# Performance work log

Measured on AMD Instinct MI355X. Metric: run time of the kernel, lower is better.

The kernel has to match this reference:

```python
import jax, jax.numpy as jnp
import numpy as np

B, S, H = 4, 2048, 1024
DECAY_RATE = 0.5  # MemoryModule decay: exp(-decay_rate * k), k=1 (most recent pattern)


def setup_inputs() -> dict:
    key = jax.random.key(0)
    ks = jax.random.split(key, 7)
    hidden_states = jax.random.normal(ks[0], (B, S, H), dtype=jnp.float32)
    # past attention pattern: valid row-stochastic attention probs [B, S, S]
    pa = jax.random.uniform(ks[1], (B, S, S), dtype=jnp.float32)
    past_attention = pa / pa.sum(-1, keepdims=True)
    scale = 1.0 / np.sqrt(H).astype(np.float32)
    Wq = jax.random.normal(ks[2], (H, H), dtype=jnp.float32) * scale
    Wk = jax.random.normal(ks[3], (H, H), dtype=jnp.float32) * scale
    Wv = jax.random.normal(ks[4], (H, H), dtype=jnp.float32) * scale
    Wm = jax.random.normal(ks[5], (H, H), dtype=jnp.float32) * scale
    w_gate = jax.random.normal(ks[6], (H,), dtype=jnp.float32) * scale
    return {"hidden_states": hidden_states, "past_attention": past_attention,
            "Wq": Wq, "Wk": Wk, "Wv": Wv, "Wm": Wm, "w_gate": w_gate}


def reference(hidden_states, past_attention, Wq, Wk, Wv, Wm, w_gate):
    h = hidden_states.shape[-1]
    inv_sqrt_h = 1.0 / (h ** 0.5)
    # QKV projections (hidden -> hidden)
    q = jnp.einsum('bsh,hd->bsd', hidden_states, Wq)
    k = jnp.einsum('bsh,hd->bsd', hidden_states, Wk)
    v = jnp.einsum('bsh,hd->bsd', hidden_states, Wv)
    # base attention scores QK^T / sqrt(H)
    scores = jnp.einsum('bqd,bkd->bqk', q, k) * inv_sqrt_h
    # --- memory bias ---
    # decayed history pattern (single most-recent entry, k=1)
    memory = past_attention * jnp.exp(jnp.float32(-DECAY_RATE * 1.0))  # [B,S,S]
    # per-token scalar gate from query
    gates = jax.nn.sigmoid(jnp.einsum('bsh,h->bs', q, w_gate))  # [B,S]
    memory_values = jnp.einsum('bqk,bkd->bqd', memory, v)        # memory @ V
    transformed = jnp.einsum('bsh,hd->bsd', memory_values, Wm)   # memory_transform (no bias)
    gated_memory = gates[..., None] * transformed
    memory_bias = jnp.einsum('bqd,bkd->bqk', gated_memory, k) * inv_sqrt_h
    # augmented attention
    probs = jax.nn.softmax(scores + memory_bias, axis=-1)
    context = jnp.einsum('bqk,bkd->bqd', probs, v)
    return context
```

## Files before the change

kernel.cpp:

```cpp
#include <hip/hip_runtime.h>
#include <hip/hip_bf16.h>

typedef __attribute__((ext_vector_type(4))) float f32x4;
typedef __attribute__((ext_vector_type(8))) __bf16 bf16x8;

__device__ __forceinline__ unsigned short f2bf(float f) {
    union { float f; unsigned u; } x; x.f = f;
    unsigned r = x.u + 0x7fffu + ((x.u >> 16) & 1u);
    return (unsigned short)(r >> 16);
}
__device__ __forceinline__ float bf2f(unsigned short b) {
    union { unsigned u; float f; } x; x.u = ((unsigned)b) << 16;
    return x.f;
}

__device__ __forceinline__ void gload16(const void* g, void* l) {
    __builtin_amdgcn_global_load_lds(
        (const __attribute__((address_space(1))) unsigned int*)g,
        (__attribute__((address_space(3))) unsigned int*)l,
        16, 0, 0);
}

template <int N> __device__ __forceinline__ void vm_wait();
template <> __device__ __forceinline__ void vm_wait<0>() { asm volatile("s_waitcnt vmcnt(0)" ::: "memory"); }
template <> __device__ __forceinline__ void vm_wait<2>() { asm volatile("s_waitcnt vmcnt(2)" ::: "memory"); }
template <> __device__ __forceinline__ void vm_wait<4>() { asm volatile("s_waitcnt vmcnt(4)" ::: "memory"); }

__global__ __launch_bounds__(256) void k_wg2(const float* __restrict__ Wq,
                                             const float* __restrict__ wg,
                                             float* __restrict__ wg2) {
    int lane = threadIdx.x & 63;
    int row = blockIdx.x * 4 + (threadIdx.x >> 6);
    const float4* a = reinterpret_cast<const float4*>(Wq + (size_t)row * 1024);
    const float4* x = reinterpret_cast<const float4*>(wg);
    float s = 0.f;
    for (int i = lane; i < 256; i += 64) {
        float4 av = a[i], bv = x[i];
        s += av.x * bv.x + av.y * bv.y + av.z * bv.z + av.w * bv.w;
    }
#pragma unroll
    for (int o = 1; o < 64; o <<= 1) s += __shfl_xor(s, o);
    if (lane == 0) wg2[row] = s;
}

__global__ __launch_bounds__(256) void k_prep(
    const float* __restrict__ hs, const float* __restrict__ pa,
    const float* __restrict__ Wq, const float* __restrict__ Wk,
    const float* __restrict__ Wv, const float* __restrict__ Wm,
    unsigned short* __restrict__ hs_bf, unsigned short* __restrict__ pa_bf,
    unsigned short* __restrict__ WT, float decay,
    const float* __restrict__ wg2, float* __restrict__ gates) {
    __shared__ float tile[32][33];
    __shared__ float red[4];
    unsigned b = blockIdx.x;
    int t = threadIdx.x;
    if (b < 16384u) {
        int i = b * 256 + t;
        float4 v = reinterpret_cast<const float4*>(pa)[i];
        union { unsigned short u[4]; uint2 q; } o;
        o.u[0] = f2bf(v.x * decay); o.u[1] = f2bf(v.y * decay);
        o.u[2] = f2bf(v.z * decay); o.u[3] = f2bf(v.w * decay);
        reinterpret_cast<uint2*>(pa_bf)[i] = o.q;
    } else if (b < 24576u) {
        unsigned row = b - 16384u;
        int i = row * 256 + t;
        float4 v = reinterpret_cast<const float4*>(hs)[i];
        union { unsigned short u[4]; uint2 q; } o;
        o.u[0] = f2bf(v.x); o.u[1] = f2bf(v.y);
        o.u[2] = f2bf(v.z); o.u[3] = f2bf(v.w);
        reinterpret_cast<uint2*>(hs_bf)[i] = o.q;
        float4 w = reinterpret_cast<const float4*>(wg2)[t];
        float s = v.x * w.x + v.y * w.y + v.z * w.z + v.w * w.w;
#pragma unroll
        for (int o2 = 1; o2 < 64; o2 <<= 1) s += __shfl_xor(s, o2);
        if ((t & 63) == 0) red[t >> 6] = s;
        __syncthreads();
        if (t == 0) {
            float ss = red[0] + red[1] + red[2] + red[3];
            gates[row] = 1.f / (1.f + __expf(-ss));
        }
    } else {
        unsigned bb = b - 24576u;
        int z = bb >> 10, rem = bb & 1023;
        int bx = rem & 31, by = rem >> 5;
        const float* src = z == 0 ? Wq : z == 1 ? Wk : z == 2 ? Wv : Wm;
        unsigned short* dst = WT + (size_t)z * 1024 * 1024;
        int lx = t & 31, ly8 = t >> 5;
        int x = bx * 32 + lx;
#pragma unroll
        for (int i = 0; i < 4; i++)
            tile[ly8 + i * 8][lx] = src[(size_t)(by * 32 + ly8 + i * 8) * 1024 + x];
        __syncthreads();
        int tx = by * 32 + lx;
#pragma unroll
        for (int i = 0; i < 4; i++)
            dst[(size_t)(bx * 32 + ly8 + i * 8) * 1024 + tx] = f2bf(tile[lx][ly8 + i * 8]);
    }
}

template <int BN>
struct Geo {
    static constexpr int WN = BN / 64;
    static constexpr int WM = 8 / WN;
    static constexpr int WROWS = 256 / WM;
    static constexpr int MF = WROWS / 16;
    static constexpr int MP = MF / 4;
    static constexpr int ASZ = 256 * 64 * 2;
    static constexpr int BSZ = BN * 64 * 2;
    static constexpr int BUFSZ = ASZ + BSZ;
};

#define GPH(BUFOFF, MB, LB, STG, VMW)                                                   \
    {                                                                                   \
        const char* aB = smem + (BUFOFF);                                               \
        const char* bB = aB + G::ASZ;                                                   \
        bf16x8 af[G::MP * 2];                                                           \
        _Pragma("unroll") for (int mm = 0; mm < G::MP; ++mm)                            \
        _Pragma("unroll") for (int kk = 0; kk < 2; ++kk) {                              \
            int rowx = wrow + ((MB) + mm) * 16 + fr;                                    \
            int slot = (kk * 4 + kq) ^ (rowx & 7);                                      \
            af[mm * 2 + kk] = *reinterpret_cast<const bf16x8*>(aB + rowx * 128 + slot * 16); \
        }                                                                               \
        if (LB) {                                                                       \
            _Pragma("unroll") for (int nn = 0; nn < 4; ++nn)                            \
            _Pragma("unroll") for (int kk = 0; kk < 2; ++kk) {                          \
                int rowx = wcol + nn * 16 + fr;                                         \
                int slot = (kk * 4 + kq) ^ (rowx & 7);                                  \
                bfrag[nn * 2 + kk] = *reinterpret_cast<const bf16x8*>(bB + rowx * 128 + slot * 16); \
            }                                                                           \
        }                                                                               \
        STG;                                                                            \
        __builtin_amdgcn_sched_barrier(0);                                              \
        VMW;                                                                            \
        __builtin_amdgcn_s_barrier();                                                   \
        asm volatile("s_waitcnt lgkmcnt(0)" ::: "memory");                              \
        __builtin_amdgcn_sched_barrier(0);                                              \
        __builtin_amdgcn_s_setprio(1);                                                  \
        _Pragma("unroll") for (int mm = 0; mm < G::MP; ++mm)                            \
        _Pragma("unroll") for (int nn = 0; nn < 4; ++nn)                                \
        _Pragma("unroll") for (int kk = 0; kk < 2; ++kk)                                \
            acc[(MB) + mm][nn] = __builtin_amdgcn_mfma_f32_16x16x32_bf16(               \
                af[mm * 2 + kk], bfrag[nn * 2 + kk], acc[(MB) + mm][nn], 0, 0, 0);      \
        __builtin_amdgcn_s_setprio(0);                                                  \
        __builtin_amdgcn_sched_barrier(0);                                              \
        __builtin_amdgcn_s_barrier();                                                   \
        __builtin_amdgcn_sched_barrier(0);                                              \
    }

template <int EPI, int BN>
__device__ __forceinline__ void gemm_body(
    char* smem,
    const unsigned short* __restrict__ A, int ldA, long long bsA,
    const unsigned short* __restrict__ Bt, int ldB, long long bsB,
    void* __restrict__ Cv, int ldC, long long bsC,
    const unsigned short* __restrict__ Qm, int ldQ,
    const float* __restrict__ gates, float alpha, int K,
    int NX, int NY, int NB, int yf) {
    using G = Geo<BN>;
    const int NT = K >> 6, NI = K >> 7;

    unsigned b = blockIdx.x;
    unsigned wg = (b & 7) * (gridDim.x >> 3) + (b >> 3);
    int xT, yT, zB;
    if (yf) {
        yT = wg % NY; unsigned r2 = wg / NY;
        xT = r2 % NX; zB = (int)(r2 / NX) % NB;
    } else {
        xT = wg % NX; unsigned r2 = wg / NX;
        yT = r2 % NY; zB = (int)(r2 / NY) % NB;
    }

    const unsigned short* Ab = A + (size_t)zB * (size_t)bsA;
    const unsigned short* Bb = Bt + (size_t)zB * (size_t)bsB;

    int t = threadIdx.x, lane = t & 63, wave = t >> 6;
    int wc = wave % G::WN, wr = wave / G::WN;
    int fr = lane & 15, kq = lane >> 4;
    int wrow = wr * G::WROWS, wcol = wc * 64;
    int trow = t >> 3, csx = (t & 7) ^ (trow & 7);
    long long rowTile = (long long)yT * 256, colTile = (long long)xT * BN;

    f32x4 acc[G::MF][4];
#pragma unroll
    for (int m = 0; m < G::MF; ++m)
#pragma unroll
        for (int n = 0; n < 4; ++n) acc[m][n] = (f32x4){0.f, 0.f, 0.f, 0.f};
    bf16x8 bfrag[8];

    auto stageA = [&](int buf, int h, int tt) {
        int kt = tt < NT ? tt : NT - 1;
#pragma unroll
        for (int rr = 0; rr < 2; ++rr) {
            const unsigned short* src =
                Ab + (size_t)(rowTile + h * 128 + rr * 64 + trow) * (size_t)ldA + kt * 64 + csx * 8;
            gload16(src, smem + buf * G::BUFSZ + h * 16384 + rr * 8192 + t * 16);
        }
    };
    auto stageB = [&](int buf, int h, int tt) {
        int kt = tt < NT ? tt : NT - 1;
        if (BN == 256) {
#pragma unroll
            for (int rr = 0; rr < 2; ++rr) {
                const unsigned short* src =
                    Bb + (size_t)(colTile + h * 128 + rr * 64 + trow) * (size_t)ldB + kt * 64 + csx * 8;
                gload16(src, smem + buf * G::BUFSZ + G::ASZ + h * 16384 + rr * 8192 + t * 16);
            }
        } else {
            const unsigned short* src =
                Bb + (size_t)(colTile + h * 64 + trow) * (size_t)ldB + kt * 64 + csx * 8;
            gload16(src, smem + buf * G::BUFSZ + G::ASZ + h * 8192 + t * 16);
        }
    };

    stageA(0, 0, 0); stageA(0, 1, 0);
    stageB(0, 0, 0); stageB(0, 1, 0);
    stageB(1, 0, 1); stageB(1, 1, 1);
    __builtin_amdgcn_sched_barrier(0);
    vm_wait<0>();
    __builtin_amdgcn_s_barrier();
    __builtin_amdgcn_sched_barrier(0);

    constexpr int VMN = (BN == 256) ? 4 : 2;
    for (int i = 0; i < NI; ++i) {
        int t1 = 2 * i + 1, t2 = 2 * i + 2, t3 = 2 * i + 3;
        GPH(0,          0,         1, stageA(1, 0, t1), (void)0);
        GPH(0,          G::MP,     0, stageA(1, 1, t1), (void)0);
        GPH(0,          2 * G::MP, 0, stageB(0, 0, t2), (void)0);
        GPH(0,          3 * G::MP, 0, stageB(0, 1, t2), vm_wait<VMN>());
        GPH(G::BUFSZ,   0,         1, stageA(0, 0, t2), (void)0);
        GPH(G::BUFSZ,   G::MP,     0, stageA(0, 1, t2), (void)0);
        GPH(G::BUFSZ,   2 * G::MP, 0, stageB(1, 0, t3), (void)0);
        GPH(G::BUFSZ,   3 * G::MP, 0, stageB(1, 1, t3), vm_wait<VMN>());
    }
    vm_wait<0>();

    long long rb0 = rowTile + wrow + kq * 4;
    long long cb0 = colTile + wcol + fr;
    if (EPI == 0) {
        unsigned short* C = (unsigned short*)Cv + (size_t)zB * (size_t)bsC;
#pragma unroll
        for (int m = 0; m < G::MF; ++m)
#pragma unroll
            for (int n = 0; n < 4; ++n)
#pragma unroll
                for (int r = 0; r < 4; ++r)
                    C[(size_t)(rb0 + m * 16 + r) * (size_t)ldC + cb0 + n * 16] =
                        f2bf(acc[m][n][r] * alpha);
    } else if (EPI == 1) {
        unsigned short* C = (unsigned short*)Cv;
#pragma unroll
        for (int m = 0; m < G::MF; ++m)
#pragma unroll
            for (int r = 0; r < 4; ++r) {
                long long row = rb0 + m * 16 + r;
                float g = gates[row];
#pragma unroll
                for (int n = 0; n < 4; ++n) {
                    long long col = cb0 + n * 16;
                    float v = (bf2f(Qm[(size_t)row * (size_t)ldQ + col]) + g * acc[m][n][r]) * alpha;
                    C[(size_t)row * (size_t)ldC + col] = f2bf(v);
                }
            }
    } else if (EPI == 4) {
        float* C = (float*)Cv + (size_t)zB * (size_t)bsC;
#pragma unroll
        for (int m = 0; m < G::MF; ++m)
#pragma unroll
            for (int r = 0; r < 4; ++r) {
                long long row = rb0 + m * 16 + r;
                const float4* pp = reinterpret_cast<const float4*>(
                    gates + ((size_t)zB * 2048 + row) * 8);
                float4 p0 = pp[0], p1 = pp[1];
                float g = 1.f / (p0.x + p0.y + p0.z + p0.w + p1.x + p1.y + p1.z + p1.w);
#pragma unroll
                for (int n = 0; n < 4; ++n)
                    C[(size_t)row * (size_t)ldC + cb0 + n * 16] = acc[m][n][r] * g;
            }
    } else if (EPI == 5) {
        unsigned short* C = (unsigned short*)Cv + (size_t)zB * (size_t)bsC;
        float* partials = (float*)gates;
        float srow[G::MF][4];
#pragma unroll
        for (int m = 0; m < G::MF; ++m)
#pragma unroll
            for (int r = 0; r < 4; ++r) srow[m][r] = 0.f;
#pragma unroll
        for (int m = 0; m < G::MF; ++m)
#pragma unroll
            for (int n = 0; n < 4; ++n)
#pragma unroll
                for (int r = 0; r < 4; ++r) {
                    float e = __expf(acc[m][n][r] * alpha);
                    C[(size_t)(rb0 + m * 16 + r) * (size_t)ldC + cb0 + n * 16] = f2bf(e);
                    srow[m][r] += e;
                }
#pragma unroll
        for (int m = 0; m < G::MF; ++m)
#pragma unroll
            for (int r = 0; r < 4; ++r) {
#pragma unroll
                for (int msk = 1; msk < 16; msk <<= 1)
                    srow[m][r] += __shfl_xor(srow[m][r], msk);
            }
        float* sums = (float*)smem;
        if (fr == 0) {
#pragma unroll
            for (int m = 0; m < G::MF; ++m)
#pragma unroll
                for (int r = 0; r < 4; ++r)
                    sums[(wrow + kq * 4 + m * 16 + r) * G::WN + wc] = srow[m][r];
        }
        __syncthreads();
        if (t < 256) {
            float s = 0.f;
#pragma unroll
            for (int j = 0; j < G::WN; ++j) s += sums[t * G::WN + j];
            partials[((size_t)zB * 2048 + (size_t)rowTile + t) * 8 + xT] = s;
        }
    }
}

#define GEMM_ARGS                                                                     \
    const unsigned short *A, int ldA, long long bsA, const unsigned short *Bt,        \
        int ldB, long long bsB, void *Cv, int ldC, long long bsC,                     \
        const unsigned short *Qm, int ldQ, const float *gates, float alpha, int K,    \
        int NX, int NY, int NB, int yf
#define GEMM_PASS A, ldA, bsA, Bt, ldB, bsB, Cv, ldC, bsC, Qm, ldQ, gates, alpha, K, NX, NY, NB, yf

__global__ __launch_bounds__(512, 2) void k_qk(GEMM_ARGS) {
    extern __shared__ char smem[];
    gemm_body<0, 256>(smem, GEMM_PASS);
}
__global__ __launch_bounds__(512, 2) void k_vt(GEMM_ARGS) {
    extern __shared__ char smem[];
    gemm_body<0, 128>(smem, GEMM_PASS);
}
__global__ __launch_bounds__(512, 2) void k_mv(GEMM_ARGS) {
    extern __shared__ char smem[];
    gemm_body<0, 128>(smem, GEMM_PASS);
}
__global__ __launch_bounds__(512, 2) void k_u(GEMM_ARGS) {
    extern __shared__ char smem[];
    gemm_body<1, 128>(smem, GEMM_PASS);
}
__global__ __launch_bounds__(512, 2) void k_logits(GEMM_ARGS) {
    extern __shared__ char smem[];
    gemm_body<5, 256>(smem, GEMM_PASS);
}
__global__ __launch_bounds__(512, 2) void k_ctx(GEMM_ARGS) {
    extern __shared__ char smem[];
    gemm_body<4, 128>(smem, GEMM_PASS);
}

extern "C" void kernel_launch(void* const* d_in, const int* in_sizes, int n_in,
                              void* d_out, int out_size, void* d_ws, size_t ws_size,
                              hipStream_t stream) {
    const float* hs = (const float*)d_in[0];
    const float* pa = (const float*)d_in[1];
    const float* Wq = (const float*)d_in[2];
    const float* Wk = (const float*)d_in[3];
    const float* Wv = (const float*)d_in[4];
    const float* Wm = (const float*)d_in[5];
    const float* wg = (const float*)d_in[6];
    float* out = (float*)d_out;

    const int B = 4, S = 2048, H = 1024;
    const size_t BS = (size_t)B * S;
    const size_t BSH = BS * H;
    const size_t BSS = (size_t)B * S * S;
    const float inv_sqrt_h = 0.03125f;
    const float decay = 0.60653065971263342f;

    char* ws = (char*)d_ws;
    size_t off = 0;
    auto take = [&](size_t bytes) {
        char* p = ws + off;
        off += (bytes + 255) & ~(size_t)255;
        return p;
    };
    unsigned short* hs_bf = (unsigned short*)take(BSH * 2);
    unsigned short* WT    = (unsigned short*)take(4ull * H * H * 2);
    float* wg2            = (float*)take(H * 4);
    float* gates          = (float*)take(BS * 4);
    unsigned short* C2    = (unsigned short*)take(BS * 2 * H * 2);
    unsigned short* v_t   = (unsigned short*)take(BSH * 2);
    unsigned short* pa_bf = (unsigned short*)take(BSS * 2);
    float* partials       = (float*)take(BS * 8 * 4);
    unsigned short* mv    = (unsigned short*)d_out;
    unsigned short* u_bf  = hs_bf;
    unsigned short* probs = pa_bf;
    unsigned short* WvT   = WT + 2ull * H * H;
    unsigned short* WmT   = WT + 3ull * H * H;

    (void)hipFuncSetAttribute((const void*)k_qk,     hipFuncAttributeMaxDynamicSharedMemorySize, 131072);
    (void)hipFuncSetAttribute((const void*)k_vt,     hipFuncAttributeMaxDynamicSharedMemorySize, 98304);
    (void)hipFuncSetAttribute((const void*)k_mv,     hipFuncAttributeMaxDynamicSharedMemorySize, 98304);
    (void)hipFuncSetAttribute((const void*)k_u,      hipFuncAttributeMaxDynamicSharedMemorySize, 98304);
    (void)hipFuncSetAttribute((const void*)k_ctx,    hipFuncAttributeMaxDynamicSharedMemorySize, 98304);
    (void)hipFuncSetAttribute((const void*)k_logits, hipFuncAttributeMaxDynamicSharedMemorySize, 131072);

    k_wg2<<<dim3(256), 256, 0, stream>>>(Wq, wg, wg2);
    k_prep<<<dim3(28672), 256, 0, stream>>>(hs, pa, Wq, Wk, Wv, Wm, hs_bf, pa_bf, WT, decay, wg2, gates);
    k_qk<<<256, 512, 131072, stream>>>(
        hs_bf, H, 0, WT, H, 0, C2, 2 * H, 0, nullptr, 0, nullptr, 1.f, H, 8, 32, 1, 0);
    k_vt<<<256, 512, 98304, stream>>>(
        WvT, H, 0, hs_bf, H, (long long)S * H, v_t, S, (long long)H * S,
        nullptr, 0, nullptr, 1.f, H, 16, 4, 4, 0);
    k_mv<<<256, 512, 98304, stream>>>(
        pa_bf, S, (long long)S * S, v_t, S, (long long)H * S, mv, H, (long long)S * H,
        nullptr, 0, nullptr, 1.f, S, 8, 8, 4, 1);
    k_u<<<256, 512, 98304, stream>>>(
        mv, H, 0, WmT, H, 0, u_bf, H, 0, C2, 2 * H, gates, inv_sqrt_h, H, 8, 32, 1, 0);
    k_logits<<<256, 512, 131072, stream>>>(
        u_bf, H, (long long)S * H, C2 + H, 2 * H, (long long)S * 2 * H,
        probs, S, (long long)S * S, nullptr, 0, partials, 1.f, H, 8, 8, 4, 1);
    k_ctx<<<256, 512, 98304, stream>>>(
        probs, S, (long long)S * S, v_t, S, (long long)H * S, out, H, (long long)S * H,
        nullptr, 0, partials, 1.f, S, 8, 8, 4, 1);
}
```

Measured before the change: 231.4 us.

## Fuse past_attention fp32-to-bf16 conversion into memory@V GEMM A-load

```diff
diff --git a/kernel.cpp b/kernel.cpp
--- a/kernel.cpp
+++ b/kernel.cpp
@@ -44,25 +44,17 @@
 }
 
 __global__ __launch_bounds__(256) void k_prep(
-    const float* __restrict__ hs, const float* __restrict__ pa,
+    const float* __restrict__ hs,
     const float* __restrict__ Wq, const float* __restrict__ Wk,
     const float* __restrict__ Wv, const float* __restrict__ Wm,
-    unsigned short* __restrict__ hs_bf, unsigned short* __restrict__ pa_bf,
-    unsigned short* __restrict__ WT, float decay,
+    unsigned short* __restrict__ hs_bf, unsigned short* __restrict__ WT,
     const float* __restrict__ wg2, float* __restrict__ gates) {
     __shared__ float tile[32][33];
     __shared__ float red[4];
     unsigned b = blockIdx.x;
     int t = threadIdx.x;
-    if (b < 16384u) {
-        int i = b * 256 + t;
-        float4 v = reinterpret_cast<const float4*>(pa)[i];
-        union { unsigned short u[4]; uint2 q; } o;
-        o.u[0] = f2bf(v.x * decay); o.u[1] = f2bf(v.y * decay);
-        o.u[2] = f2bf(v.z * decay); o.u[3] = f2bf(v.w * decay);
-        reinterpret_cast<uint2*>(pa_bf)[i] = o.q;
-    } else if (b < 24576u) {
-        unsigned row = b - 16384u;
+    if (b < 8192u) {
+        unsigned row = b;
         int i = row * 256 + t;
         float4 v = reinterpret_cast<const float4*>(hs)[i];
         union { unsigned short u[4]; uint2 q; } o;
@@ -80,7 +72,7 @@
             gates[row] = 1.f / (1.f + __expf(-ss));
         }
     } else {
-        unsigned bb = b - 24576u;
+        unsigned bb = b - 8192u;
         int z = bb >> 10, rem = bb & 1023;
         int bx = rem & 31, by = rem >> 5;
         const float* src = z == 0 ? Wq : z == 1 ? Wk : z == 2 ? Wv : Wm;
@@ -335,10 +327,6 @@
     extern __shared__ char smem[];
     gemm_body<0, 128>(smem, GEMM_PASS);
 }
-__global__ __launch_bounds__(512, 2) void k_mv(GEMM_ARGS) {
-    extern __shared__ char smem[];
-    gemm_body<0, 128>(smem, GEMM_PASS);
-}
 __global__ __launch_bounds__(512, 2) void k_u(GEMM_ARGS) {
     extern __shared__ char smem[];
     gemm_body<1, 128>(smem, GEMM_PASS);
@@ -350,6 +338,148 @@
 __global__ __launch_bounds__(512, 2) void k_ctx(GEMM_ARGS) {
     extern __shared__ char smem[];
     gemm_body<4, 128>(smem, GEMM_PASS);
+}
+
+#define MV_ASZ 32768
+#define MV_BUFSZ 49152
+
+#define MVF_PH(BUFOFF, MB, LB, STG, PW)                                             \
+    {                                                                               \
+        const char* aB = smem + (BUFOFF);                                           \
+        const char* bB = aB + MV_ASZ;                                               \
+        bf16x8 af[2];                                                               \
+        _Pragma("unroll") for (int kk = 0; kk < 2; ++kk) {                          \
+            int rowx = wrow + (MB) * 16 + fr;                                       \
+            int slot = (kk * 4 + kq) ^ (rowx & 7);                                  \
+            af[kk] = *reinterpret_cast<const bf16x8*>(aB + rowx * 128 + slot * 16); \
+        }                                                                           \
+        if (LB) {                                                                   \
+            _Pragma("unroll") for (int nn = 0; nn < 4; ++nn)                        \
+            _Pragma("unroll") for (int kk = 0; kk < 2; ++kk) {                      \
+                int rowx = wcol + nn * 16 + fr;                                     \
+                int slot = (kk * 4 + kq) ^ (rowx & 7);                              \
+                bfrag[nn * 2 + kk] = *reinterpret_cast<const bf16x8*>(bB + rowx * 128 + slot * 16); \
+            }                                                                       \
+        }                                                                           \
+        STG;                                                                        \
+        __builtin_amdgcn_sched_barrier(0);                                          \
+        PW;                                                                         \
+        __builtin_amdgcn_s_barrier();                                               \
+        asm volatile("s_waitcnt lgkmcnt(0)" ::: "memory");                          \
+        __builtin_amdgcn_sched_barrier(0);                                          \
+        __builtin_amdgcn_s_setprio(1);                                              \
+        _Pragma("unroll") for (int nn = 0; nn < 4; ++nn)                            \
+        _Pragma("unroll") for (int kk = 0; kk < 2; ++kk)                            \
+            acc[(MB)][nn] = __builtin_amdgcn_mfma_f32_16x16x32_bf16(                \
+                af[kk], bfrag[nn * 2 + kk], acc[(MB)][nn], 0, 0, 0);                \
+        __builtin_amdgcn_s_setprio(0);                                              \
+        __builtin_amdgcn_sched_barrier(0);                                          \
+        __builtin_amdgcn_s_barrier();                                               \
+        __builtin_amdgcn_sched_barrier(0);                                          \
+    }
+
+__global__ __launch_bounds__(512, 2) void k_mvf(
+    const float* __restrict__ Apa,
+    const unsigned short* __restrict__ Bt,
+    unsigned short* __restrict__ C,
+    float alpha) {
+    extern __shared__ char smem[];
+    const int NT = 32, NI = 16;
+    const int NX = 8, NY = 8, NB = 4;
+
+    unsigned b = blockIdx.x;
+    unsigned wgi = (b & 7) * (gridDim.x >> 3) + (b >> 3);
+    int yT = wgi % NY; unsigned r2 = wgi / NY;
+    int xT = r2 % NX; int zB = (int)(r2 / NX) % NB;
+
+    const float* Ab = Apa + (size_t)zB * 2048 * 2048;
+    const unsigned short* Bb = Bt + (size_t)zB * 1024 * 2048;
+
+    int t = threadIdx.x, lane = t & 63, wave = t >> 6;
+    int wc = wave & 1, wr = wave >> 1;
+    int fr = lane & 15, kq = lane >> 4;
+    int wrow = wr * 64, wcol = wc * 64;
+    int trow = t >> 3, csx = (t & 7) ^ (trow & 7);
+    long long rowTile = (long long)yT * 256, colTile = (long long)xT * 128;
+
+    f32x4 acc[4][4];
+#pragma unroll
+    for (int m = 0; m < 4; ++m)
+#pragma unroll
+        for (int n = 0; n < 4; ++n) acc[m][n] = (f32x4){0.f, 0.f, 0.f, 0.f};
+    bf16x8 bfrag[8];
+    float4 areg[8];
+
+    auto loadA = [&](int h, int tt) {
+        int kt = tt < NT ? tt : NT - 1;
+#pragma unroll
+        for (int rr = 0; rr < 2; ++rr) {
+            const float* src =
+                Ab + (size_t)(rowTile + h * 128 + rr * 64 + trow) * 2048 + kt * 64 + csx * 8;
+            areg[h * 4 + rr * 2 + 0] = *reinterpret_cast<const float4*>(src);
+            areg[h * 4 + rr * 2 + 1] = *reinterpret_cast<const float4*>(src + 4);
+        }
+    };
+    auto writeA = [&](int buf) {
+#pragma unroll
+        for (int h = 0; h < 2; ++h)
+#pragma unroll
+            for (int rr = 0; rr < 2; ++rr) {
+                float4 lo = areg[h * 4 + rr * 2], hi = areg[h * 4 + rr * 2 + 1];
+                union { unsigned short us[8]; uint4 q; } o;
+                o.us[0] = f2bf(lo.x); o.us[1] = f2bf(lo.y);
+                o.us[2] = f2bf(lo.z); o.us[3] = f2bf(lo.w);
+                o.us[4] = f2bf(hi.x); o.us[5] = f2bf(hi.y);
+                o.us[6] = f2bf(hi.z); o.us[7] = f2bf(hi.w);
+                *reinterpret_cast<uint4*>(smem + buf * MV_BUFSZ + h * 16384 + rr * 8192 + t * 16) = o.q;
+            }
+    };
+    auto stageB = [&](int buf, int h, int tt) {
+        int kt = tt < NT ? tt : NT - 1;
+        const unsigned short* src =
+            Bb + (size_t)(colTile + h * 64 + trow) * 2048 + kt * 64 + csx * 8;
+        gload16(src, smem + buf * MV_BUFSZ + MV_ASZ + h * 8192 + t * 16);
+    };
+    auto pw = [&](int buf) {
+        vm_wait<2>();
+        writeA(buf);
+        asm volatile("s_waitcnt lgkmcnt(0)" ::: "memory");
+    };
+
+    loadA(0, 0); loadA(1, 0);
+    stageB(0, 0, 0); stageB(0, 1, 0);
+    stageB(1, 0, 1); stageB(1, 1, 1);
+    __builtin_amdgcn_sched_barrier(0);
+    vm_wait<2>();
+    writeA(0);
+    asm volatile("s_waitcnt lgkmcnt(0)" ::: "memory");
+    __builtin_amdgcn_s_barrier();
+    __builtin_amdgcn_sched_barrier(0);
+
+    for (int i = 0; i < NI; ++i) {
+        int t1 = 2 * i + 1, t2 = 2 * i + 2, t3 = 2 * i + 3;
+        MVF_PH(0,         0, 1, loadA(0, t1),      (void)0);
+        MVF_PH(0,         1, 0, loadA(1, t1),      (void)0);
+        MVF_PH(0,         2, 0, stageB(0, 0, t2),  (void)0);
+        MVF_PH(0,         3, 0, stageB(0, 1, t2),  pw(1));
+        MVF_PH(MV_BUFSZ,  0, 1, loadA(0, t2),      (void)0);
+        MVF_PH(MV_BUFSZ,  1, 0, loadA(1, t2),      (void)0);
+        MVF_PH(MV_BUFSZ,  2, 0, stageB(1, 0, t3),  (void)0);
+        MVF_PH(MV_BUFSZ,  3, 0, stageB(1, 1, t3),  pw(0));
+    }
+    vm_wait<0>();
+
+    long long rb0 = rowTile + wrow + kq * 4;
+    long long cb0 = colTile + wcol + fr;
+    unsigned short* Cb = C + (size_t)zB * 2048 * 1024;
+#pragma unroll
+    for (int m = 0; m < 4; ++m)
+#pragma unroll
+        for (int n = 0; n < 4; ++n)
+#pragma unroll
+            for (int r = 0; r < 4; ++r)
+                Cb[(size_t)(rb0 + m * 16 + r) * 1024 + cb0 + n * 16] =
+                    f2bf(acc[m][n][r] * alpha);
 }
 
 extern "C" void kernel_launch(void* const* d_in, const int* in_sizes, int n_in,
@@ -384,31 +514,28 @@
     float* gates          = (float*)take(BS * 4);
     unsigned short* C2    = (unsigned short*)take(BS * 2 * H * 2);
     unsigned short* v_t   = (unsigned short*)take(BSH * 2);
-    unsigned short* pa_bf = (unsigned short*)take(BSS * 2);
+    unsigned short* probs = (unsigned short*)take(BSS * 2);
     float* partials       = (float*)take(BS * 8 * 4);
     unsigned short* mv    = (unsigned short*)d_out;
     unsigned short* u_bf  = hs_bf;
-    unsigned short* probs = pa_bf;
     unsigned short* WvT   = WT + 2ull * H * H;
     unsigned short* WmT   = WT + 3ull * H * H;
 
     (void)hipFuncSetAttribute((const void*)k_qk,     hipFuncAttributeMaxDynamicSharedMemorySize, 131072);
     (void)hipFuncSetAttribute((const void*)k_vt,     hipFuncAttributeMaxDynamicSharedMemorySize, 98304);
-    (void)hipFuncSetAttribute((const void*)k_mv,     hipFuncAttributeMaxDynamicSharedMemorySize, 98304);
+    (void)hipFuncSetAttribute((const void*)k_mvf,    hipFuncAttributeMaxDynamicSharedMemorySize, 98304);
     (void)hipFuncSetAttribute((const void*)k_u,      hipFuncAttributeMaxDynamicSharedMemorySize, 98304);
     (void)hipFuncSetAttribute((const void*)k_ctx,    hipFuncAttributeMaxDynamicSharedMemorySize, 98304);
     (void)hipFuncSetAttribute((const void*)k_logits, hipFuncAttributeMaxDynamicSharedMemorySize, 131072);
 
     k_wg2<<<dim3(256), 256, 0, stream>>>(Wq, wg, wg2);
-    k_prep<<<dim3(28672), 256, 0, stream>>>(hs, pa, Wq, Wk, Wv, Wm, hs_bf, pa_bf, WT, decay, wg2, gates);
+    k_prep<<<dim3(12288), 256, 0, stream>>>(hs, Wq, Wk, Wv, Wm, hs_bf, WT, wg2, gates);
     k_qk<<<256, 512, 131072, stream>>>(
         hs_bf, H, 0, WT, H, 0, C2, 2 * H, 0, nullptr, 0, nullptr, 1.f, H, 8, 32, 1, 0);
     k_vt<<<256, 512, 98304, stream>>>(
         WvT, H, 0, hs_bf, H, (long long)S * H, v_t, S, (long long)H * S,
         nullptr, 0, nullptr, 1.f, H, 16, 4, 4, 0);
-    k_mv<<<256, 512, 98304, stream>>>(
-        pa_bf, S, (long long)S * S, v_t, S, (long long)H * S, mv, H, (long long)S * H,
-        nullptr, 0, nullptr, 1.f, S, 8, 8, 4, 1);
+    k_mvf<<<256, 512, 98304, stream>>>(pa, v_t, mv, decay);
     k_u<<<256, 512, 98304, stream>>>(
         mv, H, 0, WmT, H, 0, u_bf, H, 0, C2, 2 * H, gates, inv_sqrt_h, H, 8, 32, 1, 0);
     k_logits<<<256, 512, 131072, stream>>>(
```

Result: slower. 264.9 us (+14.5%).
